# Performance work log

Measured on AMD Instinct MI355X. Metric: run time of the kernel, lower is better.

The kernel has to match this reference:

```python
import jax, jax.numpy as jnp
import numpy as np

INPUT_DIM = 80
ENC_DIM = 256
ATTN_DIM = 128
GRU_DIM = 256
B = 32
T_ENC = 800
T_DEC = 400


def setup_inputs() -> dict:
    key = jax.random.key(0)
    ks = jax.random.split(key, 12)
    s = 0.05
    d = {}
    d['enc_feat'] = jax.random.normal(ks[0], (B, T_ENC, ENC_DIM), jnp.float32)
    d['ground_truth'] = jax.random.normal(ks[1], (B, T_DEC, INPUT_DIM), jnp.float32)
    # GRU (PyTorch layout): weight_ih (3*G, in), weight_hh (3*G, G)
    d['W_ih'] = jax.random.normal(ks[2], (3 * GRU_DIM, INPUT_DIM + ENC_DIM), jnp.float32) * s
    d['W_hh'] = jax.random.normal(ks[3], (3 * GRU_DIM, GRU_DIM), jnp.float32) * s
    d['b_ih'] = jax.random.normal(ks[4], (3 * GRU_DIM,), jnp.float32) * s
    d['b_hh'] = jax.random.normal(ks[5], (3 * GRU_DIM,), jnp.float32) * s
    # Additive attention: v^T tanh(W_enc e + W_dec h + b)
    d['W_enc'] = jax.random.normal(ks[6], (ATTN_DIM, ENC_DIM), jnp.float32) * s
    d['W_dec'] = jax.random.normal(ks[7], (ATTN_DIM, GRU_DIM), jnp.float32) * s
    d['b_attn'] = jax.random.normal(ks[8], (ATTN_DIM,), jnp.float32) * s
    d['v_attn'] = jax.random.normal(ks[9], (ATTN_DIM,), jnp.float32) * s
    # output_trans: Linear(gru_dim + enc_feat_dim -> input_dim)
    d['W_out'] = jax.random.normal(ks[10], (INPUT_DIM, GRU_DIM + ENC_DIM), jnp.float32) * s
    d['b_out'] = jax.random.normal(ks[11], (INPUT_DIM,), jnp.float32) * s
    return d


def reference(enc_feat, ground_truth, W_ih, W_hh, b_ih, b_hh,
              W_enc, W_dec, b_attn, v_attn, W_out, b_out):
    # Teacher-forced decode (teacher_force_rate=1.0): max_step = T_dec,
    # input at each step is ground_truth[:, t, :].
    Bsz, T_enc, E = enc_feat.shape
    G = W_hh.shape[1]
    # Encoder projection for additive attention (step-invariant)
    enc_proj = jnp.einsum('bte,ae->bta', enc_feat, W_enc)  # (B, T_enc, attn_dim)

    def step(carry, x_t):
        h, ctx = carry  # h: (B,G), ctx: (B,E)
        inp = jnp.concatenate([x_t, ctx], axis=-1)  # (B, input_dim+E)
        gi = inp @ W_ih.T + b_ih
        gh = h @ W_hh.T + b_hh
        ir, iz, inn = jnp.split(gi, 3, axis=-1)
        hr, hz, hn = jnp.split(gh, 3, axis=-1)
        r = jax.nn.sigmoid(ir + hr)
        z = jax.nn.sigmoid(iz + hz)
        n = jnp.tanh(inn + r * hn)
        h_new = (1.0 - z) * n + z * h  # PyTorch GRU update
        # additive attention over encoder timesteps
        dec_proj = h_new @ W_dec.T + b_attn  # (B, attn_dim)
        scores = jnp.einsum('bta,a->bt', jnp.tanh(enc_proj + dec_proj[:, None, :]), v_attn)
        attn = jax.nn.softmax(scores, axis=-1)  # (B, T_enc)
        ctx_new = jnp.einsum('bt,bte->be', attn, enc_feat)  # (B, E)
        concat = jnp.concatenate([h_new, ctx_new], axis=-1)
        pred = jax.nn.log_softmax(concat @ W_out.T + b_out, axis=-1)
        return (h_new, ctx_new), (pred, attn)

    h0 = jnp.zeros((Bsz, G), enc_feat.dtype)
    c0 = jnp.zeros((Bsz, E), enc_feat.dtype)
    xs = jnp.swapaxes(ground_truth, 0, 1)  # (T_dec, B, input_dim)
    _, (preds, attns) = jax.lax.scan(step, (h0, c0), xs)
    pred_seq = jnp.swapaxes(preds, 0, 1)    # (B, T_dec, input_dim)
    attn_record = jnp.swapaxes(attns, 0, 1)  # (B, T_dec, T_enc)
    return pred_seq, attn_record
```

## Files before the change

### kernel.cpp

```cpp
#include <hip/hip_runtime.h>

#define BB    32
#define TDEC  400
#define TENC  800
#define EDIM  256
#define GDIM  256
#define ADIM  128
#define IDIM  80
#define G3    768
#define NSL   16
#define SLH   16
#define SLT   50
#define FSTR  16
#define EPST  144
#define ETST  58

typedef unsigned short u16;
typedef unsigned int u32;

__device__ __forceinline__ float b2f(u16 u) {
  union { u32 i; float f; } x; x.i = ((u32)u) << 16; return x.f;
}
__device__ __forceinline__ u16 f2b(float f) {
  union { float f; u32 u; } x; x.f = f;
  u32 u = x.u; u += 0x7fffu + ((u >> 16) & 1u);
  return (u16)(u >> 16);
}
__device__ __forceinline__ void ld8(const u16* p, float* w) {
  const uint4 q = *reinterpret_cast<const uint4*>(p);
  union { u32 i; float f; } c;
  c.i = q.x << 16;          w[0] = c.f;
  c.i = q.x & 0xffff0000u;  w[1] = c.f;
  c.i = q.y << 16;          w[2] = c.f;
  c.i = q.y & 0xffff0000u;  w[3] = c.f;
  c.i = q.z << 16;          w[4] = c.f;
  c.i = q.z & 0xffff0000u;  w[5] = c.f;
  c.i = q.w << 16;          w[6] = c.f;
  c.i = q.w & 0xffff0000u;  w[7] = c.f;
}
__device__ __forceinline__ void ldf8(const float* p, float* w) {
  const float4 a = *reinterpret_cast<const float4*>(p);
  const float4 b = *reinterpret_cast<const float4*>(p + 4);
  w[0] = a.x; w[1] = a.y; w[2] = a.z; w[3] = a.w;
  w[4] = b.x; w[5] = b.y; w[6] = b.z; w[7] = b.w;
}
__device__ __forceinline__ float fsigmoid(float x) {
  return __builtin_amdgcn_rcpf(1.f + __expf(-x));
}
__device__ __forceinline__ float ftanh(float x) {
  float e = __expf(2.f * x);
  return 1.f - 2.f * __builtin_amdgcn_rcpf(e + 1.f);
}
__device__ __forceinline__ void ast(float* p, float v) {
  __hip_atomic_store(p, v, __ATOMIC_RELAXED, __HIP_MEMORY_SCOPE_AGENT);
}
__device__ __forceinline__ float ald(const float* p) {
  return __hip_atomic_load(p, __ATOMIC_RELAXED, __HIP_MEMORY_SCOPE_AGENT);
}
__device__ __forceinline__ void aadd(float* p, float v) {
  (void)__hip_atomic_fetch_add(p, v, __ATOMIC_RELAXED, __HIP_MEMORY_SCOPE_AGENT);
}

__global__ __launch_bounds__(256) void k_gix(
    const float* __restrict__ gt, const float* __restrict__ W_ih,
    const float* __restrict__ b_ih, u16* __restrict__ gi_x) {
  __shared__ float sc_x[8][IDIM];
  const int tid = threadIdx.x;
  const int b = blockIdx.x / 50;
  const int t0 = (blockIdx.x % 50) * 8;
  for (int idx = tid; idx < 8 * IDIM; idx += 256) {
    int row = idx / IDIM, col = idx % IDIM;
    sc_x[row][col] = gt[((size_t)b * TDEC + t0 + row) * IDIM + col];
  }
  __syncthreads();
  for (int kk = 0; kk < 3; ++kk) {
    const int g = tid + 256 * kk;
    const float* wrow = W_ih + (size_t)g * 336;
    float acc[8] = {0,0,0,0,0,0,0,0};
    #pragma unroll 2
    for (int k8 = 0; k8 < IDIM / 8; ++k8) {
      float w[8]; ldf8(wrow + (k8 << 3), w);
      #pragma unroll
      for (int tt = 0; tt < 8; ++tt) {
        const float* x = &sc_x[tt][k8 << 3];
        acc[tt] += w[0]*x[0] + w[1]*x[1] + w[2]*x[2] + w[3]*x[3]
                 + w[4]*x[4] + w[5]*x[5] + w[6]*x[6] + w[7]*x[7];
      }
    }
    const float bias = b_ih[g];
    #pragma unroll
    for (int tt = 0; tt < 8; ++tt)
      gi_x[((size_t)b * TDEC + t0 + tt) * G3 + g] = f2b(acc[tt] + bias);
  }
}

__global__ __launch_bounds__(256) void k_encp(
    const float* __restrict__ enc_feat, const float* __restrict__ W_enc,
    u16* __restrict__ encp, u16* __restrict__ enc_bf) {
  __shared__ float sc_x[16][EDIM];
  const int tid = threadIdx.x;
  const int b = blockIdx.x / 50;
  const int te0 = (blockIdx.x % 50) * 16;
  for (int idx = tid; idx < 16 * EDIM; idx += 256) {
    int row = idx >> 8, col = idx & 255;
    sc_x[row][col] = enc_feat[((size_t)b * TENC + te0 + row) * EDIM + col];
  }
  __syncthreads();
  const int a = tid & 127;
  const int tg = tid >> 7;
  const float* wrow = W_enc + (size_t)a * EDIM;
  float acc[8] = {0,0,0,0,0,0,0,0};
  #pragma unroll 4
  for (int k8 = 0; k8 < EDIM / 8; ++k8) {
    float w[8]; ldf8(wrow + (k8 << 3), w);
    #pragma unroll
    for (int tt = 0; tt < 8; ++tt) {
      const float* x = &sc_x[tg * 8 + tt][k8 << 3];
      acc[tt] += w[0]*x[0] + w[1]*x[1] + w[2]*x[2] + w[3]*x[3]
               + w[4]*x[4] + w[5]*x[5] + w[6]*x[6] + w[7]*x[7];
    }
  }
  #pragma unroll
  for (int tt = 0; tt < 8; ++tt)
    encp[((size_t)b * TENC + te0 + tg * 8 + tt) * ADIM + a] = f2b(acc[tt]);
  for (int idx = tid; idx < 16 * EDIM; idx += 256)
    enc_bf[((size_t)b * TENC + te0) * EDIM + idx] = f2b(sc_x[idx >> 8][idx & 255]);
}

__global__ __launch_bounds__(256) void k_decode(
    const u16* __restrict__ enc_bf, const float* __restrict__ W_ih,
    const float* __restrict__ W_hh, const float* __restrict__ b_hh,
    const float* __restrict__ W_dec, const float* __restrict__ b_attn,
    const float* __restrict__ v_attn, const u16* __restrict__ gi_x,
    const u16* __restrict__ encp, float* __restrict__ stash,
    float* __restrict__ Xh, float* __restrict__ Dacc,
    float* __restrict__ Xctxacc, float* __restrict__ Xsumacc,
    int* __restrict__ flagA, int* __restrict__ flagB,
    float* __restrict__ out_attn) {
  __shared__ __align__(16) u16 encp_lds[SLT * EPST];
  __shared__ __align__(16) u16 enc_t[EDIM * ETST];
  __shared__ __align__(16) u16 sWd[128 * 26];
  __shared__ __align__(16) float sc_in[512];
  __shared__ float sc_dec[ADIM];
  __shared__ float sc_g0[48];
  __shared__ float sc_g1[48];
  __shared__ float sc_w[56];
  __shared__ float sc_v[ADIM];
  __shared__ float sc_ba[ADIM];
  __shared__ float sc_bhh[48];
  __shared__ float sc_gx[48];

  const int tid = threadIdx.x;
  const int b = blockIdx.x & 31;
  const int j = blockIdx.x >> 5;
  const int lane = tid & 63;

  u32 wctx[32], whh[32];
  #pragma unroll
  for (int i = 0; i < 32; ++i) { wctx[i] = 0u; whh[i] = 0u; }
  if (tid < 192) {
    const int r = tid >> 2, q = tid & 3;
    const int grow = (r >> 4) * 256 + SLH * j + (r & 15);
    const float2* s1 = reinterpret_cast<const float2*>(
        W_ih + (size_t)grow * 336 + 80 + q * 64);
    const float2* s2 = reinterpret_cast<const float2*>(
        W_hh + (size_t)grow * 256 + q * 64);
    #pragma unroll
    for (int i = 0; i < 32; ++i) {
      const float2 v1 = s1[i], v2 = s2[i];
      wctx[i] = (u32)f2b(v1.x) | ((u32)f2b(v1.y) << 16);
      whh[i]  = (u32)f2b(v2.x) | ((u32)f2b(v2.y) << 16);
    }
  }
  for (int idx = tid; idx < SLT * ADIM; idx += 256) {
    const int te = idx >> 7, a = idx & 127;
    encp_lds[te * EPST + a] = encp[((size_t)b * TENC + SLT * j + te) * ADIM + a];
  }
  for (int idx = tid; idx < SLT * EDIM; idx += 256) {
    const int te = idx >> 8, e = idx & 255;
    enc_t[e * ETST + te] = enc_bf[((size_t)b * TENC + SLT * j + te) * EDIM + e];
  }
  for (int idx = tid; idx < 128 * 16; idx += 256) {
    const int a = idx >> 4, k = idx & 15;
    sWd[a * 26 + k] = f2b(W_dec[(size_t)a * GDIM + SLH * j + k]);
  }
  if (tid < ADIM) { sc_v[tid] = v_attn[tid]; sc_ba[tid] = b_attn[tid]; }
  if (tid < 48) {
    const int gate = tid >> 4, i = tid & 15;
    const int grow = gate * 256 + SLH * j + i;
    const float bh = b_hh[grow];
    sc_bhh[tid] = bh;
    sc_g1[tid] = bh;
    sc_gx[tid] = b2f(gi_x[((size_t)b * TDEC + 0) * G3 + grow]);
  }
  sc_in[tid] = 0.f;
  sc_in[256 + tid] = 0.f;
  __syncthreads();

  for (int t = 0; t < TDEC; ++t) {
    const int p = t & 1;
    if (tid < 192) {
      const float* act = sc_in + ((tid & 3) << 6);
      float acc = 0.f;
      #pragma unroll
      for (int i = 0; i < 32; ++i) {
        union { u32 u; float f; } lo, hi;
        lo.u = wctx[i] << 16; hi.u = wctx[i] & 0xffff0000u;
        acc += lo.f * act[2 * i] + hi.f * act[2 * i + 1];
      }
      acc += __shfl_xor(acc, 1);
      acc += __shfl_xor(acc, 2);
      if ((tid & 3) == 0) sc_g0[tid >> 2] = acc + sc_gx[tid >> 2];
    }
    __syncthreads();
    if (tid < 64) {
      float hval = 0.f;
      if (lane < SLH) {
        const float gr = sc_g0[lane] + sc_g1[lane];
        const float gz = sc_g0[SLH + lane] + sc_g1[SLH + lane];
        const float rr = fsigmoid(gr);
        const float zz = fsigmoid(gz);
        const float nn = ftanh(sc_g0[2 * SLH + lane] + rr * sc_g1[2 * SLH + lane]);
        const float hp = sc_in[256 + SLH * j + lane];
        hval = (1.f - zz) * nn + zz * hp;
        ast(&Xh[b * GDIM + SLH * j + lane], hval);
      }
      float hn16[16];
      #pragma unroll
      for (int k = 0; k < 16; ++k) hn16[k] = __shfl(hval, k);
      #pragma unroll
      for (int r2 = 0; r2 < 2; ++r2) {
        const int a = lane + 64 * r2;
        const u32* wp = reinterpret_cast<const u32*>(&sWd[a * 26]);
        float acc = 0.f;
        #pragma unroll
        for (int k2 = 0; k2 < 8; ++k2) {
          const u32 w2 = wp[k2];
          union { u32 u; float f; } lo, hi;
          lo.u = w2 << 16; hi.u = w2 & 0xffff0000u;
          acc += lo.f * hn16[2 * k2] + hi.f * hn16[2 * k2 + 1];
        }
        aadd(&Dacc[(b * 2 + p) * ADIM + a], acc);
      }
    }
    __syncthreads();
    if (tid == 0)
      __hip_atomic_store(&flagA[(b * NSL + j) * FSTR], t + 1, __ATOMIC_RELAXED,
                         __HIP_MEMORY_SCOPE_AGENT);
    if (tid < NSL) {
      const int* fp = &flagA[(b * NSL + tid) * FSTR];
      while (__hip_atomic_load(fp, __ATOMIC_RELAXED,
                               __HIP_MEMORY_SCOPE_AGENT) < t + 1)
        __builtin_amdgcn_s_sleep(1);
    }
    __syncthreads();
    sc_in[256 + tid] = ald(&Xh[b * GDIM + tid]);
    if (tid < ADIM)
      sc_dec[tid] = ald(&Dacc[(b * 2 + p) * ADIM + tid]) + sc_ba[tid];
    if (tid < 16) ast(&Xctxacc[(b * 2 + (1 - p)) * EDIM + j * 16 + tid], 0.f);
    if (j == 0) {
      if (tid >= 128) ast(&Dacc[(b * 2 + (1 - p)) * ADIM + (tid - 128)], 0.f);
      if (tid == 16) ast(&Xsumacc[(b * 2 + (1 - p)) * FSTR], 0.f);
    }
    __syncthreads();
    if (tid < 192) {
      const float* act = sc_in + 256 + ((tid & 3) << 6);
      float acc = 0.f;
      #pragma unroll
      for (int i = 0; i < 32; ++i) {
        union { u32 u; float f; } lo, hi;
        lo.u = whh[i] << 16; hi.u = whh[i] & 0xffff0000u;
        acc += lo.f * act[2 * i] + hi.f * act[2 * i + 1];
      }
      acc += __shfl_xor(acc, 1);
      acc += __shfl_xor(acc, 2);
      if ((tid & 3) == 0) sc_g1[tid >> 2] = acc + sc_bhh[tid >> 2];
    }
    if (tid < 200) {
      const int te = tid >> 2, q4 = tid & 3;
      const u16* ep = &encp_lds[te * EPST + q4 * 32];
      const float* dp = sc_dec + q4 * 32;
      const float* vp = sc_v + q4 * 32;
      float s = 0.f;
      #pragma unroll
      for (int k8 = 0; k8 < 4; ++k8) {
        float w[8]; ld8(ep + (k8 << 3), w);
        #pragma unroll
        for (int i = 0; i < 8; ++i) {
          const int a = (k8 << 3) + i;
          s += ftanh(w[i] + dp[a]) * vp[a];
        }
      }
      s += __shfl_xor(s, 1);
      s += __shfl_xor(s, 2);
      if (q4 == 0) sc_w[te] = __expf(s);
    } else if (tid < 248) {
      const int gl = tid - 200;
      const int grow = (gl >> 4) * 256 + SLH * j + (gl & 15);
      const int tn = (t + 1 < TDEC) ? t + 1 : t;
      sc_gx[gl] = b2f(gi_x[((size_t)b * TDEC + tn) * G3 + grow]);
    }
    if (tid >= 248)
      stash[((size_t)b * TDEC + t) * 512 + SLH * j + (tid - 248) * 2] = 0.f;
    __syncthreads();
    if (tid < SLH)
      stash[((size_t)b * TDEC + t) * 512 + SLH * j + tid] =
          sc_in[256 + SLH * j + tid];
    if (tid < 64) {
      float v = (tid < SLT) ? sc_w[tid] : 0.f;
      #pragma unroll
      for (int off = 1; off < 64; off <<= 1) v += __shfl_xor(v, off);
      if (tid == 0) aadd(&Xsumacc[(b * 2 + p) * FSTR], v);
    }
    {
      const u32* et = reinterpret_cast<const u32*>(&enc_t[tid * ETST]);
      float pc = 0.f;
      #pragma unroll
      for (int k2 = 0; k2 < 25; ++k2) {
        const u32 w2 = et[k2];
        union { u32 u; float f; } lo, hi;
        lo.u = w2 << 16; hi.u = w2 & 0xffff0000u;
        pc += sc_w[2 * k2] * lo.f + sc_w[2 * k2 + 1] * hi.f;
      }
      aadd(&Xctxacc[(b * 2 + p) * EDIM + tid], pc);
    }
    __syncthreads();
    if (tid == 0)
      __hip_atomic_store(&flagB[(b * NSL + j) * FSTR], t + 1, __ATOMIC_RELAXED,
                         __HIP_MEMORY_SCOPE_AGENT);
    if (tid < NSL) {
      const int* fp = &flagB[(b * NSL + tid) * FSTR];
      while (__hip_atomic_load(fp, __ATOMIC_RELAXED,
                               __HIP_MEMORY_SCOPE_AGENT) < t + 1)
        __builtin_amdgcn_s_sleep(1);
    }
    __syncthreads();
    {
      float s0 = 0.f;
      if ((tid & 63) == 0) s0 = ald(&Xsumacc[(b * 2 + p) * FSTR]);
      const float S = __shfl(s0, 0);
      const float c = ald(&Xctxacc[(b * 2 + p) * EDIM + tid]);
      const float invS = __builtin_amdgcn_rcpf(S);
      const float cv = c * invS;
      sc_in[tid] = cv;
      if (j == 0) stash[((size_t)b * TDEC + t) * 512 + EDIM + tid] = cv;
      if (tid < SLT)
        out_attn[((size_t)b * TDEC + t) * TENC + SLT * j + tid] =
            sc_w[tid] * invS;
    }
    __syncthreads();
  }
}

__global__ __launch_bounds__(256) void k_pred(
    const float* __restrict__ stash, const float* __restrict__ W_out,
    const float* __restrict__ b_out, float* __restrict__ out_pred) {
  __shared__ float sc_s[4][512];
  __shared__ float sc_lp[2][4][IDIM];
  __shared__ float sc_l[4][IDIM];
  __shared__ float sc_lse[4];
  const int tid = threadIdx.x;
  const int b = blockIdx.x / 100;
  const int t0 = (blockIdx.x % 100) * 4;
  for (int idx = tid; idx < 4 * 512; idx += 256)
    sc_s[idx >> 9][idx & 511] = stash[((size_t)b * TDEC + t0) * 512 + idx];
  __syncthreads();
  const int o = tid & 127, kh = tid >> 7;
  if (o < IDIM) {
    const float* wrow = W_out + (size_t)o * 512 + kh * 256;
    float acc[4] = {0,0,0,0};
    #pragma unroll 4
    for (int k8 = 0; k8 < 32; ++k8) {
      float w[8]; ldf8(wrow + (k8 << 3), w);
      #pragma unroll
      for (int tt = 0; tt < 4; ++tt) {
        const float* x = &sc_s[tt][kh * 256 + (k8 << 3)];
        acc[tt] += w[0]*x[0] + w[1]*x[1] + w[2]*x[2] + w[3]*x[3]
                 + w[4]*x[4] + w[5]*x[5] + w[6]*x[6] + w[7]*x[7];
      }
    }
    #pragma unroll
    for (int tt = 0; tt < 4; ++tt) sc_lp[kh][tt][o] = acc[tt];
  }
  __syncthreads();
  if (tid < IDIM) {
    const float bb = b_out[tid];
    #pragma unroll
    for (int tt = 0; tt < 4; ++tt)
      sc_l[tt][tid] = sc_lp[0][tt][tid] + sc_lp[1][tt][tid] + bb;
  }
  __syncthreads();
  {
    const int w = tid >> 6, lane = tid & 63;
    const float a0 = sc_l[w][lane];
    const float a1 = (lane < IDIM - 64) ? sc_l[w][lane + 64] : -1e30f;
    float m = fmaxf(a0, a1);
    #pragma unroll
    for (int off = 1; off < 64; off <<= 1) m = fmaxf(m, __shfl_xor(m, off));
    float e = __expf(a0 - m) + ((lane < IDIM - 64) ? __expf(a1 - m) : 0.f);
    #pragma unroll
    for (int off = 1; off < 64; off <<= 1) e += __shfl_xor(e, off);
    if (lane == 0) sc_lse[w] = m + __logf(e);
  }
  __syncthreads();
  for (int idx = tid; idx < 4 * IDIM; idx += 256) {
    const int tt = idx / IDIM, oo = idx % IDIM;
    out_pred[((size_t)b * TDEC + t0 + tt) * IDIM + oo] =
        sc_l[tt][oo] - sc_lse[tt];
  }
}

extern "C" void kernel_launch(void* const* d_in, const int* in_sizes, int n_in,
                              void* d_out, int out_size, void* d_ws, size_t ws_size,
                              hipStream_t stream) {
  const float* enc_feat = (const float*)d_in[0];
  const float* gt       = (const float*)d_in[1];
  const float* W_ih     = (const float*)d_in[2];
  const float* W_hh     = (const float*)d_in[3];
  const float* b_ih     = (const float*)d_in[4];
  const float* b_hh     = (const float*)d_in[5];
  const float* W_enc    = (const float*)d_in[6];
  const float* W_dec    = (const float*)d_in[7];
  const float* b_attn   = (const float*)d_in[8];
  const float* v_attn   = (const float*)d_in[9];
  const float* W_out    = (const float*)d_in[10];
  const float* b_out    = (const float*)d_in[11];
  float* out_pred = (float*)d_out;
  float* out_attn = out_pred + (size_t)BB * TDEC * IDIM;

  char* ws = (char*)d_ws;
  size_t off = 0;
  u16* gi_x   = (u16*)(ws + off);   off += (size_t)BB * TDEC * G3 * 2;
  u16* encp   = (u16*)(ws + off);   off += (size_t)BB * TENC * ADIM * 2;
  u16* enc_bf = (u16*)(ws + off);   off += (size_t)BB * TENC * EDIM * 2;
  float* stash= (float*)(ws + off); off += (size_t)BB * TDEC * 512 * 4;
  float* Xh   = (float*)(ws + off); off += (size_t)BB * GDIM * 4;
  char* zbase = ws + off;
  int* flagA    = (int*)(ws + off);   off += (size_t)BB * NSL * FSTR * 4;
  int* flagB    = (int*)(ws + off);   off += (size_t)BB * NSL * FSTR * 4;
  float* Dacc   = (float*)(ws + off); off += (size_t)BB * 2 * ADIM * 4;
  float* Xctxacc= (float*)(ws + off); off += (size_t)BB * 2 * EDIM * 4;
  float* Xsumacc= (float*)(ws + off); off += (size_t)BB * 2 * FSTR * 4;
  const size_t zbytes = (size_t)(ws + off - zbase);

  hipMemsetAsync(zbase, 0, zbytes, stream);

  hipLaunchKernelGGL(k_gix, dim3(BB * 50), dim3(256), 0, stream,
                     gt, W_ih, b_ih, gi_x);
  hipLaunchKernelGGL(k_encp, dim3(BB * 50), dim3(256), 0, stream,
                     enc_feat, W_enc, encp, enc_bf);
  hipLaunchKernelGGL(k_decode, dim3(BB * NSL), dim3(256), 0, stream,
                     enc_bf, W_ih, W_hh, b_hh, W_dec, b_attn, v_attn,
                     gi_x, encp, stash, Xh, Dacc, Xctxacc, Xsumacc,
                     flagA, flagB, out_attn);
  hipLaunchKernelGGL(k_pred, dim3(BB * 100), dim3(256), 0, stream,
                     stash, W_out, b_out, out_pred);
}
```

Baseline: 3.460 ms.

## Replace flag barriers and atomic adds with sentinel-tagged per-slice partial buffers

Cross-block synchronization in the persistent decode kernel moves from counter flags plus atomic fetch-add accumulators to double-buffered per-slice partial arrays. Each value is written as a plain store, and readers poll until it differs from a NaN sentinel. Readers then sum the 16 slice partials locally, which removes the two flag barriers per step, the atomic contention and the separate zeroing pass. The W_hh matvec is moved after the context computation, and the W_dec weights are packed as bf16 pairs. The scheme relies on the relaxed-store/load ordering and the sentinel resets being correct, and it adds more polling loads per thread.

```diff
diff --git a/kernel.cpp b/kernel.cpp
--- a/kernel.cpp
+++ b/kernel.cpp
@@ -11,9 +11,10 @@
 #define NSL   16
 #define SLH   16
 #define SLT   50
-#define FSTR  16
-#define EPST  144
+#define EPST  136
 #define ETST  58
+#define CAN   0x7FC00BADu
+#define CSTR  272
 
 typedef unsigned short u16;
 typedef unsigned int u32;
@@ -54,11 +55,20 @@
 __device__ __forceinline__ void ast(float* p, float v) {
   __hip_atomic_store(p, v, __ATOMIC_RELAXED, __HIP_MEMORY_SCOPE_AGENT);
 }
-__device__ __forceinline__ float ald(const float* p) {
-  return __hip_atomic_load(p, __ATOMIC_RELAXED, __HIP_MEMORY_SCOPE_AGENT);
-}
-__device__ __forceinline__ void aadd(float* p, float v) {
-  (void)__hip_atomic_fetch_add(p, v, __ATOMIC_RELAXED, __HIP_MEMORY_SCOPE_AGENT);
+__device__ __forceinline__ void asti(int* p, u32 v) {
+  __hip_atomic_store(p, (int)v, __ATOMIC_RELAXED, __HIP_MEMORY_SCOPE_AGENT);
+}
+__device__ __forceinline__ u32 aldi(const int* p) {
+  return (u32)__hip_atomic_load(p, __ATOMIC_RELAXED, __HIP_MEMORY_SCOPE_AGENT);
+}
+
+__global__ __launch_bounds__(256) void k_init(int* __restrict__ XhP,
+                                              int* __restrict__ XdP,
+                                              int* __restrict__ XcP) {
+  const int i = blockIdx.x * 256 + threadIdx.x;
+  if (i < 2 * BB * GDIM) XhP[i] = (int)CAN;
+  if (i < 2 * BB * NSL * ADIM) XdP[i] = (int)CAN;
+  if (i < 2 * BB * NSL * CSTR) XcP[i] = (int)CAN;
 }
 
 __global__ __launch_bounds__(256) void k_gix(
@@ -127,20 +137,20 @@
     enc_bf[((size_t)b * TENC + te0) * EDIM + idx] = f2b(sc_x[idx >> 8][idx & 255]);
 }
 
-__global__ __launch_bounds__(256) void k_decode(
-    const u16* __restrict__ enc_bf, const float* __restrict__ W_ih,
-    const float* __restrict__ W_hh, const float* __restrict__ b_hh,
-    const float* __restrict__ W_dec, const float* __restrict__ b_attn,
-    const float* __restrict__ v_attn, const u16* __restrict__ gi_x,
-    const u16* __restrict__ encp, float* __restrict__ stash,
-    float* __restrict__ Xh, float* __restrict__ Dacc,
-    float* __restrict__ Xctxacc, float* __restrict__ Xsumacc,
-    int* __restrict__ flagA, int* __restrict__ flagB,
-    float* __restrict__ out_attn) {
+__global__ __launch_bounds__(256, 2) void k_decode(
+    const float* __restrict__ W_ih, const float* __restrict__ W_hh,
+    const float* __restrict__ b_hh, const float* __restrict__ W_dec,
+    const float* __restrict__ b_attn, const float* __restrict__ v_attn,
+    const u16* __restrict__ gi_x, const u16* __restrict__ encp,
+    const u16* __restrict__ enc_bf, float* __restrict__ stash,
+    float* __restrict__ XhP, float* __restrict__ XdP,
+    float* __restrict__ XcP, float* __restrict__ out_attn) {
   __shared__ __align__(16) u16 encp_lds[SLT * EPST];
   __shared__ __align__(16) u16 enc_t[EDIM * ETST];
-  __shared__ __align__(16) u16 sWd[128 * 26];
-  __shared__ __align__(16) float sc_in[512];
+  __shared__ u32 sWdp[128 * 9];
+  __shared__ __align__(16) float sc_h[256];
+  __shared__ float sc_ing[4][68];
+  __shared__ float sc_inh[4][68];
   __shared__ float sc_dec[ADIM];
   __shared__ float sc_g0[48];
   __shared__ float sc_g1[48];
@@ -149,6 +159,7 @@
   __shared__ float sc_ba[ADIM];
   __shared__ float sc_bhh[48];
   __shared__ float sc_gx[48];
+  __shared__ float sc_xs[NSL];
 
   const int tid = threadIdx.x;
   const int b = blockIdx.x & 31;
@@ -172,6 +183,12 @@
       whh[i]  = (u32)f2b(v2.x) | ((u32)f2b(v2.y) << 16);
     }
   }
+  for (int idx = tid; idx < 128 * 8; idx += 256) {
+    const int a = idx >> 3, k2 = idx & 7;
+    const float2 v = *reinterpret_cast<const float2*>(
+        W_dec + (size_t)a * GDIM + SLH * j + 2 * k2);
+    sWdp[a * 9 + k2] = (u32)f2b(v.x) | ((u32)f2b(v.y) << 16);
+  }
   for (int idx = tid; idx < SLT * ADIM; idx += 256) {
     const int te = idx >> 7, a = idx & 127;
     encp_lds[te * EPST + a] = encp[((size_t)b * TENC + SLT * j + te) * ADIM + a];
@@ -179,10 +196,6 @@
   for (int idx = tid; idx < SLT * EDIM; idx += 256) {
     const int te = idx >> 8, e = idx & 255;
     enc_t[e * ETST + te] = enc_bf[((size_t)b * TENC + SLT * j + te) * EDIM + e];
-  }
-  for (int idx = tid; idx < 128 * 16; idx += 256) {
-    const int a = idx >> 4, k = idx & 15;
-    sWd[a * 26 + k] = f2b(W_dec[(size_t)a * GDIM + SLH * j + k]);
   }
   if (tid < ADIM) { sc_v[tid] = v_attn[tid]; sc_ba[tid] = b_attn[tid]; }
   if (tid < 48) {
@@ -193,14 +206,18 @@
     sc_g1[tid] = bh;
     sc_gx[tid] = b2f(gi_x[((size_t)b * TDEC + 0) * G3 + grow]);
   }
-  sc_in[tid] = 0.f;
-  sc_in[256 + tid] = 0.f;
+  sc_h[tid] = 0.f;
+  sc_ing[tid >> 6][tid & 63] = 0.f;
+  sc_inh[tid >> 6][tid & 63] = 0.f;
   __syncthreads();
 
   for (int t = 0; t < TDEC; ++t) {
     const int p = t & 1;
+    float* XhPp = XhP + (p * BB + b) * GDIM;
+    float* XdPp = XdP + ((p * BB + b) * NSL + j) * ADIM;
+    float* XcPp = XcP + ((p * BB + b) * NSL) * CSTR;
     if (tid < 192) {
-      const float* act = sc_in + ((tid & 3) << 6);
+      const float* act = &sc_ing[tid & 3][0];
       float acc = 0.f;
       #pragma unroll
       for (int i = 0; i < 32; ++i) {
@@ -221,9 +238,9 @@
         const float rr = fsigmoid(gr);
         const float zz = fsigmoid(gz);
         const float nn = ftanh(sc_g0[2 * SLH + lane] + rr * sc_g1[2 * SLH + lane]);
-        const float hp = sc_in[256 + SLH * j + lane];
+        const float hp = sc_h[SLH * j + lane];
         hval = (1.f - zz) * nn + zz * hp;
-        ast(&Xh[b * GDIM + SLH * j + lane], hval);
+        ast(&XhPp[SLH * j + lane], hval);
       }
       float hn16[16];
       #pragma unroll
@@ -231,7 +248,7 @@
       #pragma unroll
       for (int r2 = 0; r2 < 2; ++r2) {
         const int a = lane + 64 * r2;
-        const u32* wp = reinterpret_cast<const u32*>(&sWd[a * 26]);
+        const u32* wp = &sWdp[a * 9];
         float acc = 0.f;
         #pragma unroll
         for (int k2 = 0; k2 < 8; ++k2) {
@@ -240,42 +257,45 @@
           lo.u = w2 << 16; hi.u = w2 & 0xffff0000u;
           acc += lo.f * hn16[2 * k2] + hi.f * hn16[2 * k2 + 1];
         }
-        aadd(&Dacc[(b * 2 + p) * ADIM + a], acc);
-      }
-    }
+        ast(&XdPp[a], acc);
+      }
+    }
+    {
+      const int* hp_ = (const int*)&XhPp[tid];
+      const int* dbase = (const int*)(XdP + ((p * BB + b) * NSL) * ADIM
+                                      + (tid & 127));
+      u32 hu = CAN;
+      u32 gotd = (tid < ADIM) ? 0u : 0xFFFFu;
+      float dsum = 0.f;
+      for (;;) {
+        bool done = true;
+        if (hu == CAN) { hu = aldi(hp_); if (hu == CAN) done = false; }
+        if (gotd != 0xFFFFu) {
+          #pragma unroll
+          for (int jj = 0; jj < NSL; ++jj) {
+            if (!(gotd & (1u << jj))) {
+              const u32 u = aldi(dbase + jj * ADIM);
+              if (u != CAN) {
+                union { u32 uu; float f; } v; v.uu = u;
+                dsum += v.f;
+                gotd |= (1u << jj);
+              }
+            }
+          }
+          if (gotd != 0xFFFFu) done = false;
+        }
+        if (done) break;
+        __builtin_amdgcn_s_sleep(1);
+      }
+      union { u32 uu; float f; } hv; hv.uu = hu;
+      sc_h[tid] = hv.f;
+      sc_inh[tid >> 6][tid & 63] = hv.f;
+      if (tid < ADIM) sc_dec[tid] = dsum + sc_ba[tid];
+    }
+    asti((int*)&XcP[(((1 - p) * BB + b) * NSL + j) * CSTR + tid], CAN);
+    if (tid == 0)
+      asti((int*)&XcP[(((1 - p) * BB + b) * NSL + j) * CSTR + 256], CAN);
     __syncthreads();
-    if (tid == 0)
-      __hip_atomic_store(&flagA[(b * NSL + j) * FSTR], t + 1, __ATOMIC_RELAXED,
-                         __HIP_MEMORY_SCOPE_AGENT);
-    if (tid < NSL) {
-      const int* fp = &flagA[(b * NSL + tid) * FSTR];
-      while (__hip_atomic_load(fp, __ATOMIC_RELAXED,
-                               __HIP_MEMORY_SCOPE_AGENT) < t + 1)
-        __builtin_amdgcn_s_sleep(1);
-    }
-    __syncthreads();
-    sc_in[256 + tid] = ald(&Xh[b * GDIM + tid]);
-    if (tid < ADIM)
-      sc_dec[tid] = ald(&Dacc[(b * 2 + p) * ADIM + tid]) + sc_ba[tid];
-    if (tid < 16) ast(&Xctxacc[(b * 2 + (1 - p)) * EDIM + j * 16 + tid], 0.f);
-    if (j == 0) {
-      if (tid >= 128) ast(&Dacc[(b * 2 + (1 - p)) * ADIM + (tid - 128)], 0.f);
-      if (tid == 16) ast(&Xsumacc[(b * 2 + (1 - p)) * FSTR], 0.f);
-    }
-    __syncthreads();
-    if (tid < 192) {
-      const float* act = sc_in + 256 + ((tid & 3) << 6);
-      float acc = 0.f;
-      #pragma unroll
-      for (int i = 0; i < 32; ++i) {
-        union { u32 u; float f; } lo, hi;
-        lo.u = whh[i] << 16; hi.u = whh[i] & 0xffff0000u;
-        acc += lo.f * act[2 * i] + hi.f * act[2 * i + 1];
-      }
-      acc += __shfl_xor(acc, 1);
-      acc += __shfl_xor(acc, 2);
-      if ((tid & 3) == 0) sc_g1[tid >> 2] = acc + sc_bhh[tid >> 2];
-    }
     if (tid < 200) {
       const int te = tid >> 2, q4 = tid & 3;
       const u16* ep = &encp_lds[te * EPST + q4 * 32];
@@ -300,17 +320,12 @@
       const int tn = (t + 1 < TDEC) ? t + 1 : t;
       sc_gx[gl] = b2f(gi_x[((size_t)b * TDEC + tn) * G3 + grow]);
     }
-    if (tid >= 248)
-      stash[((size_t)b * TDEC + t) * 512 + SLH * j + (tid - 248) * 2] = 0.f;
     __syncthreads();
-    if (tid < SLH)
-      stash[((size_t)b * TDEC + t) * 512 + SLH * j + tid] =
-          sc_in[256 + SLH * j + tid];
     if (tid < 64) {
       float v = (tid < SLT) ? sc_w[tid] : 0.f;
       #pragma unroll
       for (int off = 1; off < 64; off <<= 1) v += __shfl_xor(v, off);
-      if (tid == 0) aadd(&Xsumacc[(b * 2 + p) * FSTR], v);
+      if (tid == 0) ast(&XcPp[j * CSTR + 256], v);
     }
     {
       const u32* et = reinterpret_cast<const u32*>(&enc_t[tid * ETST]);
@@ -322,31 +337,65 @@
         lo.u = w2 << 16; hi.u = w2 & 0xffff0000u;
         pc += sc_w[2 * k2] * lo.f + sc_w[2 * k2 + 1] * hi.f;
       }
-      aadd(&Xctxacc[(b * 2 + p) * EDIM + tid], pc);
-    }
-    __syncthreads();
-    if (tid == 0)
-      __hip_atomic_store(&flagB[(b * NSL + j) * FSTR], t + 1, __ATOMIC_RELAXED,
-                         __HIP_MEMORY_SCOPE_AGENT);
+      ast(&XcPp[j * CSTR + tid], pc);
+    }
+    if (tid < 192) {
+      const float* act = &sc_inh[tid & 3][0];
+      float acc = 0.f;
+      #pragma unroll
+      for (int i = 0; i < 32; ++i) {
+        union { u32 u; float f; } lo, hi;
+        lo.u = whh[i] << 16; hi.u = whh[i] & 0xffff0000u;
+        acc += lo.f * act[2 * i] + hi.f * act[2 * i + 1];
+      }
+      acc += __shfl_xor(acc, 1);
+      acc += __shfl_xor(acc, 2);
+      if ((tid & 3) == 0) sc_g1[tid >> 2] = acc + sc_bhh[tid >> 2];
+    }
     if (tid < NSL) {
-      const int* fp = &flagB[(b * NSL + tid) * FSTR];
-      while (__hip_atomic_load(fp, __ATOMIC_RELAXED,
-                               __HIP_MEMORY_SCOPE_AGENT) < t + 1)
-        __builtin_amdgcn_s_sleep(1);
+      const int* sp = (const int*)&XcPp[tid * CSTR + 256];
+      u32 u = aldi(sp);
+      while (u == CAN) { __builtin_amdgcn_s_sleep(1); u = aldi(sp); }
+      union { u32 uu; float f; } sv; sv.uu = u;
+      sc_xs[tid] = sv.f;
+    }
+    float c = 0.f;
+    {
+      u32 got = 0;
+      while (got != 0xFFFFu) {
+        #pragma unroll
+        for (int jj = 0; jj < NSL; ++jj) {
+          if (!(got & (1u << jj))) {
+            const u32 u = aldi((const int*)&XcPp[jj * CSTR + tid]);
+            if (u != CAN) {
+              union { u32 uu; float f; } v; v.uu = u;
+              c += v.f;
+              got |= (1u << jj);
+            }
+          }
+        }
+        if (got != 0xFFFFu) __builtin_amdgcn_s_sleep(1);
+      }
     }
     __syncthreads();
     {
-      float s0 = 0.f;
-      if ((tid & 63) == 0) s0 = ald(&Xsumacc[(b * 2 + p) * FSTR]);
-      const float S = __shfl(s0, 0);
-      const float c = ald(&Xctxacc[(b * 2 + p) * EDIM + tid]);
+      float S = 0.f;
+      #pragma unroll
+      for (int jj = 0; jj < NSL; ++jj) S += sc_xs[jj];
       const float invS = __builtin_amdgcn_rcpf(S);
       const float cv = c * invS;
-      sc_in[tid] = cv;
-      if (j == 0) stash[((size_t)b * TDEC + t) * 512 + EDIM + tid] = cv;
+      sc_ing[tid >> 6][tid & 63] = cv;
+      if (j == 0) stash[((size_t)b * TDEC + t) * 512 + 256 + tid] = cv;
+      if (tid < SLH)
+        stash[((size_t)b * TDEC + t) * 512 + SLH * j + tid] = sc_h[SLH * j + tid];
       if (tid < SLT)
         out_attn[((size_t)b * TDEC + t) * TENC + SLT * j + tid] =
             sc_w[tid] * invS;
+      if (tid < SLH) asti((int*)&XhPp[SLH * j + tid], CAN);
+      if (tid < 64) {
+        asti((int*)&XdPp[tid], CAN);
+        asti((int*)&XdPp[tid + 64], CAN);
+      }
     }
     __syncthreads();
   }
@@ -434,25 +483,19 @@
   u16* encp   = (u16*)(ws + off);   off += (size_t)BB * TENC * ADIM * 2;
   u16* enc_bf = (u16*)(ws + off);   off += (size_t)BB * TENC * EDIM * 2;
   float* stash= (float*)(ws + off); off += (size_t)BB * TDEC * 512 * 4;
-  float* Xh   = (float*)(ws + off); off += (size_t)BB * GDIM * 4;
-  char* zbase = ws + off;
-  int* flagA    = (int*)(ws + off);   off += (size_t)BB * NSL * FSTR * 4;
-  int* flagB    = (int*)(ws + off);   off += (size_t)BB * NSL * FSTR * 4;
-  float* Dacc   = (float*)(ws + off); off += (size_t)BB * 2 * ADIM * 4;
-  float* Xctxacc= (float*)(ws + off); off += (size_t)BB * 2 * EDIM * 4;
-  float* Xsumacc= (float*)(ws + off); off += (size_t)BB * 2 * FSTR * 4;
-  const size_t zbytes = (size_t)(ws + off - zbase);
-
-  hipMemsetAsync(zbase, 0, zbytes, stream);
-
+  float* XhP  = (float*)(ws + off); off += (size_t)2 * BB * GDIM * 4;
+  float* XdP  = (float*)(ws + off); off += (size_t)2 * BB * NSL * ADIM * 4;
+  float* XcP  = (float*)(ws + off); off += (size_t)2 * BB * NSL * CSTR * 4;
+
+  hipLaunchKernelGGL(k_init, dim3((2 * BB * NSL * CSTR + 255) / 256), dim3(256),
+                     0, stream, (int*)XhP, (int*)XdP, (int*)XcP);
   hipLaunchKernelGGL(k_gix, dim3(BB * 50), dim3(256), 0, stream,
                      gt, W_ih, b_ih, gi_x);
   hipLaunchKernelGGL(k_encp, dim3(BB * 50), dim3(256), 0, stream,
                      enc_feat, W_enc, encp, enc_bf);
   hipLaunchKernelGGL(k_decode, dim3(BB * NSL), dim3(256), 0, stream,
-                     enc_bf, W_ih, W_hh, b_hh, W_dec, b_attn, v_attn,
-                     gi_x, encp, stash, Xh, Dacc, Xctxacc, Xsumacc,
-                     flagA, flagB, out_attn);
+                     W_ih, W_hh, b_hh, W_dec, b_attn, v_attn,
+                     gi_x, encp, enc_bf, stash, XhP, XdP, XcP, out_attn);
   hipLaunchKernelGGL(k_pred, dim3(BB * 100), dim3(256), 0, stream,
                      stash, W_out, b_out, out_pred);
 }
```

Measured after the change: 5.868 ms. +69.6%, slower.

## Bank cross-block atomic accumulators and move W_hh matvec after attention phase

Applied to the files above, without the earlier changes.

The shared accumulators for decoder projection, context and softmax sum are split into four banks indexed by slice id, which spreads same-address atomic adds across four locations; readers sum the four banks. The W_hh gate matvec moves out of its own phase into the attention/context phase, which removes one __syncthreads per step. Zeroing of the next buffers and the hidden-state stash writes are redistributed across blocks. LDS layouts change (padded packed W_dec, per-quarter input buffers, EPST stride) and launch bounds ask for two blocks per CU. The cost is more global reads per step and a larger workspace.

```diff
diff --git a/kernel.cpp b/kernel.cpp
--- a/kernel.cpp
+++ b/kernel.cpp
@@ -12,7 +12,7 @@
 #define SLH   16
 #define SLT   50
 #define FSTR  16
-#define EPST  144
+#define EPST  136
 #define ETST  58
 
 typedef unsigned short u16;
@@ -127,20 +127,22 @@
     enc_bf[((size_t)b * TENC + te0) * EDIM + idx] = f2b(sc_x[idx >> 8][idx & 255]);
 }
 
-__global__ __launch_bounds__(256) void k_decode(
-    const u16* __restrict__ enc_bf, const float* __restrict__ W_ih,
-    const float* __restrict__ W_hh, const float* __restrict__ b_hh,
-    const float* __restrict__ W_dec, const float* __restrict__ b_attn,
-    const float* __restrict__ v_attn, const u16* __restrict__ gi_x,
-    const u16* __restrict__ encp, float* __restrict__ stash,
+__global__ __launch_bounds__(256, 2) void k_decode(
+    const float* __restrict__ W_ih, const float* __restrict__ W_hh,
+    const float* __restrict__ b_hh, const float* __restrict__ W_dec,
+    const float* __restrict__ b_attn, const float* __restrict__ v_attn,
+    const u16* __restrict__ gi_x, const u16* __restrict__ encp,
+    const u16* __restrict__ enc_bf, float* __restrict__ stash,
     float* __restrict__ Xh, float* __restrict__ Dacc,
     float* __restrict__ Xctxacc, float* __restrict__ Xsumacc,
     int* __restrict__ flagA, int* __restrict__ flagB,
     float* __restrict__ out_attn) {
   __shared__ __align__(16) u16 encp_lds[SLT * EPST];
   __shared__ __align__(16) u16 enc_t[EDIM * ETST];
-  __shared__ __align__(16) u16 sWd[128 * 26];
-  __shared__ __align__(16) float sc_in[512];
+  __shared__ u32 sWdp[128 * 9];
+  __shared__ __align__(16) float sc_h[256];
+  __shared__ float sc_ing[4][68];
+  __shared__ float sc_inh[4][68];
   __shared__ float sc_dec[ADIM];
   __shared__ float sc_g0[48];
   __shared__ float sc_g1[48];
@@ -149,11 +151,13 @@
   __shared__ float sc_ba[ADIM];
   __shared__ float sc_bhh[48];
   __shared__ float sc_gx[48];
+  __shared__ float sc_xs[4];
 
   const int tid = threadIdx.x;
   const int b = blockIdx.x & 31;
   const int j = blockIdx.x >> 5;
   const int lane = tid & 63;
+  const int bank = j & 3;
 
   u32 wctx[32], whh[32];
   #pragma unroll
@@ -172,6 +176,12 @@
       whh[i]  = (u32)f2b(v2.x) | ((u32)f2b(v2.y) << 16);
     }
   }
+  for (int idx = tid; idx < 128 * 8; idx += 256) {
+    const int a = idx >> 3, k2 = idx & 7;
+    const float2 v = *reinterpret_cast<const float2*>(
+        W_dec + (size_t)a * GDIM + SLH * j + 2 * k2);
+    sWdp[a * 9 + k2] = (u32)f2b(v.x) | ((u32)f2b(v.y) << 16);
+  }
   for (int idx = tid; idx < SLT * ADIM; idx += 256) {
     const int te = idx >> 7, a = idx & 127;
     encp_lds[te * EPST + a] = encp[((size_t)b * TENC + SLT * j + te) * ADIM + a];
@@ -179,10 +189,6 @@
   for (int idx = tid; idx < SLT * EDIM; idx += 256) {
     const int te = idx >> 8, e = idx & 255;
     enc_t[e * ETST + te] = enc_bf[((size_t)b * TENC + SLT * j + te) * EDIM + e];
-  }
-  for (int idx = tid; idx < 128 * 16; idx += 256) {
-    const int a = idx >> 4, k = idx & 15;
-    sWd[a * 26 + k] = f2b(W_dec[(size_t)a * GDIM + SLH * j + k]);
   }
   if (tid < ADIM) { sc_v[tid] = v_attn[tid]; sc_ba[tid] = b_attn[tid]; }
   if (tid < 48) {
@@ -193,14 +199,15 @@
     sc_g1[tid] = bh;
     sc_gx[tid] = b2f(gi_x[((size_t)b * TDEC + 0) * G3 + grow]);
   }
-  sc_in[tid] = 0.f;
-  sc_in[256 + tid] = 0.f;
+  sc_h[tid] = 0.f;
+  sc_ing[tid >> 6][tid & 63] = 0.f;
+  sc_inh[tid >> 6][tid & 63] = 0.f;
   __syncthreads();
 
   for (int t = 0; t < TDEC; ++t) {
     const int p = t & 1;
     if (tid < 192) {
-      const float* act = sc_in + ((tid & 3) << 6);
+      const float* act = &sc_ing[tid & 3][0];
       float acc = 0.f;
       #pragma unroll
       for (int i = 0; i < 32; ++i) {
@@ -221,7 +228,7 @@
         const float rr = fsigmoid(gr);
         const float zz = fsigmoid(gz);
         const float nn = ftanh(sc_g0[2 * SLH + lane] + rr * sc_g1[2 * SLH + lane]);
-        const float hp = sc_in[256 + SLH * j + lane];
+        const float hp = sc_h[SLH * j + lane];
         hval = (1.f - zz) * nn + zz * hp;
         ast(&Xh[b * GDIM + SLH * j + lane], hval);
       }
@@ -231,7 +238,7 @@
       #pragma unroll
       for (int r2 = 0; r2 < 2; ++r2) {
         const int a = lane + 64 * r2;
-        const u32* wp = reinterpret_cast<const u32*>(&sWd[a * 26]);
+        const u32* wp = &sWdp[a * 9];
         float acc = 0.f;
         #pragma unroll
         for (int k2 = 0; k2 < 8; ++k2) {
@@ -240,7 +247,7 @@
           lo.u = w2 << 16; hi.u = w2 & 0xffff0000u;
           acc += lo.f * hn16[2 * k2] + hi.f * hn16[2 * k2 + 1];
         }
-        aadd(&Dacc[(b * 2 + p) * ADIM + a], acc);
+        aadd(&Dacc[((p * BB + b) * 4 + bank) * ADIM + a], acc);
       }
     }
     __syncthreads();
@@ -254,28 +261,29 @@
         __builtin_amdgcn_s_sleep(1);
     }
     __syncthreads();
-    sc_in[256 + tid] = ald(&Xh[b * GDIM + tid]);
-    if (tid < ADIM)
-      sc_dec[tid] = ald(&Dacc[(b * 2 + p) * ADIM + tid]) + sc_ba[tid];
-    if (tid < 16) ast(&Xctxacc[(b * 2 + (1 - p)) * EDIM + j * 16 + tid], 0.f);
-    if (j == 0) {
-      if (tid >= 128) ast(&Dacc[(b * 2 + (1 - p)) * ADIM + (tid - 128)], 0.f);
-      if (tid == 16) ast(&Xsumacc[(b * 2 + (1 - p)) * FSTR], 0.f);
-    }
-    __syncthreads();
-    if (tid < 192) {
-      const float* act = sc_in + 256 + ((tid & 3) << 6);
-      float acc = 0.f;
-      #pragma unroll
-      for (int i = 0; i < 32; ++i) {
-        union { u32 u; float f; } lo, hi;
-        lo.u = whh[i] << 16; hi.u = whh[i] & 0xffff0000u;
-        acc += lo.f * act[2 * i] + hi.f * act[2 * i + 1];
-      }
-      acc += __shfl_xor(acc, 1);
-      acc += __shfl_xor(acc, 2);
-      if ((tid & 3) == 0) sc_g1[tid >> 2] = acc + sc_bhh[tid >> 2];
-    }
+    {
+      const float hv = ald(&Xh[b * GDIM + tid]);
+      sc_h[tid] = hv;
+      sc_inh[tid >> 6][tid & 63] = hv;
+      if (j == 0) stash[((size_t)b * TDEC + t) * 512 + tid] = hv;
+    }
+    if (tid < ADIM) {
+      float d = sc_ba[tid];
+      #pragma unroll
+      for (int k = 0; k < 4; ++k)
+        d += ald(&Dacc[((p * BB + b) * 4 + k) * ADIM + tid]);
+      sc_dec[tid] = d;
+    }
+    if (tid < 64) {
+      const int w = j * 64 + tid;
+      ast(&Xctxacc[(((1 - p) * BB + b) * 4 + (w >> 8)) * EDIM + (w & 255)], 0.f);
+    } else if (tid < 96) {
+      const int w = j * 32 + (tid - 64);
+      ast(&Dacc[(((1 - p) * BB + b) * 4 + (w >> 7)) * ADIM + (w & 127)], 0.f);
+    } else if (tid == 96 && j < 4) {
+      ast(&Xsumacc[(((1 - p) * BB + b) * 4 + j) * FSTR], 0.f);
+    }
+    __syncthreads();
     if (tid < 200) {
       const int te = tid >> 2, q4 = tid & 3;
       const u16* ep = &encp_lds[te * EPST + q4 * 32];
@@ -300,17 +308,12 @@
       const int tn = (t + 1 < TDEC) ? t + 1 : t;
       sc_gx[gl] = b2f(gi_x[((size_t)b * TDEC + tn) * G3 + grow]);
     }
-    if (tid >= 248)
-      stash[((size_t)b * TDEC + t) * 512 + SLH * j + (tid - 248) * 2] = 0.f;
-    __syncthreads();
-    if (tid < SLH)
-      stash[((size_t)b * TDEC + t) * 512 + SLH * j + tid] =
-          sc_in[256 + SLH * j + tid];
+    __syncthreads();
     if (tid < 64) {
       float v = (tid < SLT) ? sc_w[tid] : 0.f;
       #pragma unroll
       for (int off = 1; off < 64; off <<= 1) v += __shfl_xor(v, off);
-      if (tid == 0) aadd(&Xsumacc[(b * 2 + p) * FSTR], v);
+      if (tid == 0) aadd(&Xsumacc[((p * BB + b) * 4 + bank) * FSTR], v);
     }
     {
       const u32* et = reinterpret_cast<const u32*>(&enc_t[tid * ETST]);
@@ -322,7 +325,20 @@
         lo.u = w2 << 16; hi.u = w2 & 0xffff0000u;
         pc += sc_w[2 * k2] * lo.f + sc_w[2 * k2 + 1] * hi.f;
       }
-      aadd(&Xctxacc[(b * 2 + p) * EDIM + tid], pc);
+      aadd(&Xctxacc[((p * BB + b) * 4 + bank) * EDIM + tid], pc);
+    }
+    if (tid < 192) {
+      const float* act = &sc_inh[tid & 3][0];
+      float acc = 0.f;
+      #pragma unroll
+      for (int i = 0; i < 32; ++i) {
+        union { u32 u; float f; } lo, hi;
+        lo.u = whh[i] << 16; hi.u = whh[i] & 0xffff0000u;
+        acc += lo.f * act[2 * i] + hi.f * act[2 * i + 1];
+      }
+      acc += __shfl_xor(acc, 1);
+      acc += __shfl_xor(acc, 2);
+      if ((tid & 3) == 0) sc_g1[tid >> 2] = acc + sc_bhh[tid >> 2];
     }
     __syncthreads();
     if (tid == 0)
@@ -333,17 +349,19 @@
       while (__hip_atomic_load(fp, __ATOMIC_RELAXED,
                                __HIP_MEMORY_SCOPE_AGENT) < t + 1)
         __builtin_amdgcn_s_sleep(1);
+      if (tid < 4) sc_xs[tid] = ald(&Xsumacc[((p * BB + b) * 4 + tid) * FSTR]);
     }
     __syncthreads();
     {
-      float s0 = 0.f;
-      if ((tid & 63) == 0) s0 = ald(&Xsumacc[(b * 2 + p) * FSTR]);
-      const float S = __shfl(s0, 0);
-      const float c = ald(&Xctxacc[(b * 2 + p) * EDIM + tid]);
+      const float S = sc_xs[0] + sc_xs[1] + sc_xs[2] + sc_xs[3];
+      float c = 0.f;
+      #pragma unroll
+      for (int k = 0; k < 4; ++k)
+        c += ald(&Xctxacc[((p * BB + b) * 4 + k) * EDIM + tid]);
       const float invS = __builtin_amdgcn_rcpf(S);
       const float cv = c * invS;
-      sc_in[tid] = cv;
-      if (j == 0) stash[((size_t)b * TDEC + t) * 512 + EDIM + tid] = cv;
+      sc_ing[tid >> 6][tid & 63] = cv;
+      if (j == 0) stash[((size_t)b * TDEC + t) * 512 + 256 + tid] = cv;
       if (tid < SLT)
         out_attn[((size_t)b * TDEC + t) * TENC + SLT * j + tid] =
             sc_w[tid] * invS;
@@ -438,9 +456,9 @@
   char* zbase = ws + off;
   int* flagA    = (int*)(ws + off);   off += (size_t)BB * NSL * FSTR * 4;
   int* flagB    = (int*)(ws + off);   off += (size_t)BB * NSL * FSTR * 4;
-  float* Dacc   = (float*)(ws + off); off += (size_t)BB * 2 * ADIM * 4;
-  float* Xctxacc= (float*)(ws + off); off += (size_t)BB * 2 * EDIM * 4;
-  float* Xsumacc= (float*)(ws + off); off += (size_t)BB * 2 * FSTR * 4;
+  float* Dacc   = (float*)(ws + off); off += (size_t)BB * 2 * 4 * ADIM * 4;
+  float* Xctxacc= (float*)(ws + off); off += (size_t)BB * 2 * 4 * EDIM * 4;
+  float* Xsumacc= (float*)(ws + off); off += (size_t)BB * 2 * 4 * FSTR * 4;
   const size_t zbytes = (size_t)(ws + off - zbase);
 
   hipMemsetAsync(zbase, 0, zbytes, stream);
@@ -450,8 +468,8 @@
   hipLaunchKernelGGL(k_encp, dim3(BB * 50), dim3(256), 0, stream,
                      enc_feat, W_enc, encp, enc_bf);
   hipLaunchKernelGGL(k_decode, dim3(BB * NSL), dim3(256), 0, stream,
-                     enc_bf, W_ih, W_hh, b_hh, W_dec, b_attn, v_attn,
-                     gi_x, encp, stash, Xh, Dacc, Xctxacc, Xsumacc,
+                     W_ih, W_hh, b_hh, W_dec, b_attn, v_attn,
+                     gi_x, encp, enc_bf, stash, Xh, Dacc, Xctxacc, Xsumacc,
                      flagA, flagB, out_attn);
   hipLaunchKernelGGL(k_pred, dim3(BB * 100), dim3(256), 0, stream,
                      stash, W_out, b_out, out_pred);
```

Measured after the change: 3.391 ms. 2.0% less time.
